# Kernel tuning notes

Hardware: AMD Instinct MI355X
Metric: run time of the kernel (lower is better)

## Reference

```python
import jax, jax.numpy as jnp
import numpy as np

MARGIN = 0.01
B, L, P, D = 32, 1024, 8, 256  # splits, candidates per split, positives per split, embed dim


def _l2_normalize(x):
    # matches torch F.normalize(dim=-1) with eps clamp
    n = jnp.linalg.norm(x, axis=-1, keepdims=True)
    return x / jnp.maximum(n, 1e-12)


def setup_inputs() -> dict:
    key = jax.random.key(0)
    k1, k2, k3 = jax.random.split(key, 3)
    sent_embeddings = jax.random.normal(k1, (B, L, D), dtype=jnp.float32)
    query_embeddings = jax.random.normal(k2, (B, D), dtype=jnp.float32)
    # distinct positive indices per split (random permutation prefix)
    pos_idx = jnp.argsort(jax.random.uniform(k3, (B, L)), axis=1)[:, :P].astype(jnp.int64)
    return {
        "sent_embeddings": sent_embeddings,
        "query_embeddings": query_embeddings,
        "pos_idx": pos_idx,
        "splits": L,
    }


def reference(sent_embeddings, query_embeddings, pos_idx, splits):
    # per-candidate cosine similarity to its split's query: [B, L]
    e = _l2_normalize(sent_embeddings)
    q = _l2_normalize(query_embeddings)
    sim = jnp.einsum('bld,bd->bl', e, q)

    b, l = sim.shape
    pos_mask = jnp.zeros((b, l), dtype=bool).at[jnp.arange(b)[:, None], pos_idx].set(True)
    neg_mask = ~pos_mask

    # pairwise hinge: relu(neg_sim - pos_sim + margin), pos on axis 1, neg on axis 2
    pair = jax.nn.relu(sim[:, None, :] - sim[:, :, None] + MARGIN)  # [B, L, L]
    w = (pos_mask[:, :, None] & neg_mask[:, None, :]).astype(sim.dtype)
    total = (pos_mask.sum(axis=1) * neg_mask.sum(axis=1)).sum().astype(sim.dtype)
    loss = (pair * w).sum() / total
    return loss
```

## Files before the change

### kernel.cpp

```cpp
#include <hip/hip_runtime.h>
#include <math.h>

#define BB 32
#define LL 1024
#define PP 8
#define DD 256
#define MARGIN_F 0.01f
#define TOTAL_PAIRS 260096.0f
#define NBLK 1024

__global__ __launch_bounds__(256) void main_kernel(const float* __restrict__ sent,
                                                   const float* __restrict__ query,
                                                   const int* __restrict__ pos_idx,
                                                   float* __restrict__ partial) {
    const int blk   = blockIdx.x;
    const int b     = blk >> 5;
    const int chunk = blk & 31;
    const int tid   = threadIdx.x;
    const int g     = tid >> 4;
    const int seg   = tid & 15;

    const float* qr = query + (size_t)b * DD;

    float4 qv[4];
#pragma unroll
    for (int k = 0; k < 4; ++k)
        qv[k] = *reinterpret_cast<const float4*>(qr + (k * 16 + seg) * 4);

    const int l0 = chunk * 32 + g;
    const int l1 = chunk * 32 + 16 + g;
    const float* x0 = sent + ((size_t)(b * LL + l0)) * DD;
    const float* x1 = sent + ((size_t)(b * LL + l1)) * DD;
    float4 xv0[4], xv1[4];
#pragma unroll
    for (int k = 0; k < 4; ++k) {
        xv0[k] = *reinterpret_cast<const float4*>(x0 + (k * 16 + seg) * 4);
        xv1[k] = *reinterpret_cast<const float4*>(x1 + (k * 16 + seg) * 4);
    }

    __shared__ float ltpos[PP];
    __shared__ int   lpid[PP];
    float4 pv[4];
    int prow = 0;
    if (g < PP) {
        prow = pos_idx[b * PP + g];
#pragma unroll
        for (int k = 0; k < 4; ++k)
            pv[k] = *reinterpret_cast<const float4*>(sent + ((size_t)(b * LL + prow)) * DD + (k * 16 + seg) * 4);
    }

    float nq = 0.f;
#pragma unroll
    for (int k = 0; k < 4; ++k)
        nq += qv[k].x * qv[k].x + qv[k].y * qv[k].y + qv[k].z * qv[k].z + qv[k].w * qv[k].w;
#pragma unroll
    for (int off = 8; off > 0; off >>= 1) nq += __shfl_xor(nq, off, 16);
    const float qiv = 1.0f / fmaxf(sqrtf(nq), 1e-12f);

    if (g < PP) {
        float dot = 0.f, nx = 0.f;
#pragma unroll
        for (int k = 0; k < 4; ++k) {
            dot += pv[k].x * qv[k].x + pv[k].y * qv[k].y + pv[k].z * qv[k].z + pv[k].w * qv[k].w;
            nx  += pv[k].x * pv[k].x + pv[k].y * pv[k].y + pv[k].z * pv[k].z + pv[k].w * pv[k].w;
        }
#pragma unroll
        for (int off = 8; off > 0; off >>= 1) {
            dot += __shfl_xor(dot, off, 16);
            nx  += __shfl_xor(nx,  off, 16);
        }
        if (seg == 0) {
            ltpos[g] = (dot * qiv) / fmaxf(sqrtf(nx), 1e-12f) - MARGIN_F;
            lpid[g]  = prow;
        }
    }
    __syncthreads();

    float tpos[PP];
    int   pidr[PP];
#pragma unroll
    for (int p = 0; p < PP; ++p) { tpos[p] = ltpos[p]; pidr[p] = lpid[p]; }

    float d0 = 0.f, n0 = 0.f, d1 = 0.f, n1 = 0.f;
#pragma unroll
    for (int k = 0; k < 4; ++k) {
        d0 += xv0[k].x * qv[k].x + xv0[k].y * qv[k].y + xv0[k].z * qv[k].z + xv0[k].w * qv[k].w;
        n0 += xv0[k].x * xv0[k].x + xv0[k].y * xv0[k].y + xv0[k].z * xv0[k].z + xv0[k].w * xv0[k].w;
        d1 += xv1[k].x * qv[k].x + xv1[k].y * qv[k].y + xv1[k].z * qv[k].z + xv1[k].w * qv[k].w;
        n1 += xv1[k].x * xv1[k].x + xv1[k].y * xv1[k].y + xv1[k].z * xv1[k].z + xv1[k].w * xv1[k].w;
    }
#pragma unroll
    for (int off = 8; off > 0; off >>= 1) {
        d0 += __shfl_xor(d0, off, 16);
        n0 += __shfl_xor(n0, off, 16);
        d1 += __shfl_xor(d1, off, 16);
        n1 += __shfl_xor(n1, off, 16);
    }

    float acc = 0.f;
    if (seg == 0) {
        const float s0 = (d0 * qiv) / fmaxf(sqrtf(n0), 1e-12f);
        const float s1 = (d1 * qiv) / fmaxf(sqrtf(n1), 1e-12f);
        bool p0 = false, p1 = false;
#pragma unroll
        for (int p = 0; p < PP; ++p) {
            p0 |= (l0 == pidr[p]);
            p1 |= (l1 == pidr[p]);
        }
        if (!p0) {
#pragma unroll
            for (int p = 0; p < PP; ++p) acc += fmaxf(s0 - tpos[p], 0.f);
        }
        if (!p1) {
#pragma unroll
            for (int p = 0; p < PP; ++p) acc += fmaxf(s1 - tpos[p], 0.f);
        }
    }

#pragma unroll
    for (int off = 32; off > 0; off >>= 1) acc += __shfl_xor(acc, off, 64);
    __shared__ float wsum[4];
    if ((tid & 63) == 0) wsum[tid >> 6] = acc;
    __syncthreads();
    if (tid == 0) partial[blk] = wsum[0] + wsum[1] + wsum[2] + wsum[3];
}

__global__ __launch_bounds__(256) void final_kernel(const float* __restrict__ partial,
                                                    float* __restrict__ out) {
    const int tid = threadIdx.x;
    const float4 v = *reinterpret_cast<const float4*>(partial + tid * 4);
    float s = v.x + v.y + v.z + v.w;
#pragma unroll
    for (int off = 32; off > 0; off >>= 1) s += __shfl_xor(s, off, 64);
    __shared__ float wsum[4];
    if ((tid & 63) == 0) wsum[tid >> 6] = s;
    __syncthreads();
    if (tid == 0) out[0] = (wsum[0] + wsum[1] + wsum[2] + wsum[3]) / TOTAL_PAIRS;
}

extern "C" void kernel_launch(void* const* d_in, const int* in_sizes, int n_in,
                              void* d_out, int out_size, void* d_ws, size_t ws_size,
                              hipStream_t stream) {
    const float* sent  = (const float*)d_in[0];
    const float* query = (const float*)d_in[1];
    const int*   pidx  = (const int*)d_in[2];
    float* out = (float*)d_out;
    float* partial = (float*)d_ws;

    main_kernel <<<NBLK, 256, 0, stream>>>(sent, query, pidx, partial);
    final_kernel<<<1, 256, 0, stream>>>(partial, out);
}
```

Baseline: 13.24 us.

## Fuse final reduction into main kernel via last-block atomic ticket

Removes the separate final reduction kernel. Each block now publishes its partial sum with an atomic exchange and takes a ticket with an atomic add, and the last block to arrive sums all partials and writes the loss. Blocks are doubled to 512 threads so only 512 blocks are launched. This trades a kernel launch for a memset plus atomics, and relies on an asm trick to order the partial store before the ticket increment rather than on a proper fence.

```diff
diff --git a/kernel.cpp b/kernel.cpp
--- a/kernel.cpp
+++ b/kernel.cpp
@@ -7,15 +7,17 @@
 #define DD 256
 #define MARGIN_F 0.01f
 #define TOTAL_PAIRS 260096.0f
-#define NBLK 1024
+#define NBLK 512
 
-__global__ __launch_bounds__(256) void main_kernel(const float* __restrict__ sent,
+__global__ __launch_bounds__(512) void main_kernel(const float* __restrict__ sent,
                                                    const float* __restrict__ query,
                                                    const int* __restrict__ pos_idx,
-                                                   float* __restrict__ partial) {
+                                                   float* __restrict__ partial,
+                                                   unsigned* __restrict__ ticket,
+                                                   float* __restrict__ out) {
     const int blk   = blockIdx.x;
-    const int b     = blk >> 5;
-    const int chunk = blk & 31;
+    const int b     = blk >> 4;
+    const int chunk = blk & 15;
     const int tid   = threadIdx.x;
     const int g     = tid >> 4;
     const int seg   = tid & 15;
@@ -27,8 +29,8 @@
     for (int k = 0; k < 4; ++k)
         qv[k] = *reinterpret_cast<const float4*>(qr + (k * 16 + seg) * 4);
 
-    const int l0 = chunk * 32 + g;
-    const int l1 = chunk * 32 + 16 + g;
+    const int l0 = chunk * 64 + g;
+    const int l1 = chunk * 64 + 32 + g;
     const float* x0 = sent + ((size_t)(b * LL + l0)) * DD;
     const float* x1 = sent + ((size_t)(b * LL + l1)) * DD;
     float4 xv0[4], xv1[4];
@@ -119,23 +121,38 @@
 
 #pragma unroll
     for (int off = 32; off > 0; off >>= 1) acc += __shfl_xor(acc, off, 64);
-    __shared__ float wsum[4];
+    __shared__ float wsum[8];
     if ((tid & 63) == 0) wsum[tid >> 6] = acc;
     __syncthreads();
-    if (tid == 0) partial[blk] = wsum[0] + wsum[1] + wsum[2] + wsum[3];
-}
 
-__global__ __launch_bounds__(256) void final_kernel(const float* __restrict__ partial,
-                                                    float* __restrict__ out) {
-    const int tid = threadIdx.x;
-    const float4 v = *reinterpret_cast<const float4*>(partial + tid * 4);
-    float s = v.x + v.y + v.z + v.w;
+    __shared__ int lastflag;
+    if (tid == 0) {
+        float p = 0.f;
+#pragma unroll
+        for (int w = 0; w < 8; ++w) p += wsum[w];
+        const float old = __hip_atomic_exchange(&partial[blk], p,
+                                                __ATOMIC_RELAXED, __HIP_MEMORY_SCOPE_AGENT);
+        unsigned oz;
+        asm volatile("v_and_b32 %0, 0, %1" : "=v"(oz) : "v"(__float_as_uint(old)));
+        const unsigned t = __hip_atomic_fetch_add(ticket, 1u + oz,
+                                                  __ATOMIC_RELAXED, __HIP_MEMORY_SCOPE_AGENT);
+        lastflag = (t == (unsigned)(NBLK - 1));
+    }
+    __syncthreads();
+    if (!lastflag) return;
+
+    float s = __hip_atomic_load(&partial[tid], __ATOMIC_RELAXED, __HIP_MEMORY_SCOPE_AGENT);
 #pragma unroll
     for (int off = 32; off > 0; off >>= 1) s += __shfl_xor(s, off, 64);
-    __shared__ float wsum[4];
-    if ((tid & 63) == 0) wsum[tid >> 6] = s;
+    __shared__ float fsum[8];
+    if ((tid & 63) == 0) fsum[tid >> 6] = s;
     __syncthreads();
-    if (tid == 0) out[0] = (wsum[0] + wsum[1] + wsum[2] + wsum[3]) / TOTAL_PAIRS;
+    if (tid == 0) {
+        float total = 0.f;
+#pragma unroll
+        for (int w = 0; w < 8; ++w) total += fsum[w];
+        out[0] = total / TOTAL_PAIRS;
+    }
 }
 
 extern "C" void kernel_launch(void* const* d_in, const int* in_sizes, int n_in,
@@ -145,8 +162,10 @@
     const float* query = (const float*)d_in[1];
     const int*   pidx  = (const int*)d_in[2];
     float* out = (float*)d_out;
-    float* partial = (float*)d_ws;
 
-    main_kernel <<<NBLK, 256, 0, stream>>>(sent, query, pidx, partial);
-    final_kernel<<<1, 256, 0, stream>>>(partial, out);
+    unsigned* ticket  = (unsigned*)d_ws;
+    float*    partial = (float*)d_ws + 64;
+
+    hipMemsetAsync(d_ws, 0, 4, stream);
+    main_kernel<<<NBLK, 512, 0, stream>>>(sent, query, pidx, partial, ticket, out);
 }
```

Result: slower. 20.73 us (+56.5%).
